# Kernel optimization log

Measured on AMD Instinct MI355X. Metric: run time of the kernel, lower is better.

## Reference

```python
import jax, jax.numpy as jnp
import numpy as np

UNITS = 128  # rnn_units hardcoded in the module


def setup_inputs() -> dict:
    key = jax.random.key(0)
    k1, k2, k3 = jax.random.split(key, 3)
    B, T, F = 256, 1024, 128  # feature dim must equal UNITS (shared cell across both layers)
    inputs = jax.random.normal(k1, (B, T, F), dtype=jnp.float32)
    # Keras LSTMCell params, gate order i|f|g|o; SHARED by both stacked layers
    # because StackedRNNCells([cell]*2) reuses the same cell object.
    W = jax.random.normal(k2, (F, 4 * UNITS), dtype=jnp.float32) * 0.05   # kernel
    U = jax.random.normal(k3, (UNITS, 4 * UNITS), dtype=jnp.float32) * 0.05  # recurrent_kernel
    b = jnp.zeros((4 * UNITS,), dtype=jnp.float32)  # bias
    return {"inputs": inputs, "W": W, "U": U, "b": b}


def _lstm_cell(x, h, c, W, U, b):
    # z: [B, 4*UNITS]; Keras gate order i, f, g(candidate), o
    z = x @ W + h @ U + b
    i, f, g, o = jnp.split(z, 4, axis=-1)
    i = jax.nn.sigmoid(i)
    f = jax.nn.sigmoid(f)
    g = jnp.tanh(g)
    o = jax.nn.sigmoid(o)
    c_new = f * c + i * g
    h_new = o * jnp.tanh(c_new)
    return h_new, c_new


def reference(inputs, W, U, b):
    B, T, F = inputs.shape
    z0 = jnp.zeros((B, UNITS), dtype=inputs.dtype)

    def step(carry, x_t):
        h1, c1, h2, c2 = carry
        h1, c1 = _lstm_cell(x_t, h1, c1, W, U, b)   # layer 1
        h2, c2 = _lstm_cell(h1, h2, c2, W, U, b)    # layer 2 (shared weights)
        return (h1, c1, h2, c2), None

    (h1, c1, h2, c2), _ = jax.lax.scan(step, (z0, z0, z0, z0), jnp.swapaxes(inputs, 0, 1))
    outputs = h2                                    # last-step output (return_sequences=False)
    init_state = jnp.zeros(inputs.shape, dtype=inputs.dtype)  # tf.zeros(inputs.shape)
    final_state = c1  # source unpacks `outputs, _, h2, _, _` -> 2nd flat state = layer-1 cell state
    return (outputs, init_state, final_state)
```

## Files before the change

### kernel.cpp

```cpp
#include <hip/hip_runtime.h>


typedef _Float16 f16;
typedef _Float16 f16x2 __attribute__((ext_vector_type(2)));
typedef _Float16 f16x8 __attribute__((ext_vector_type(8)));
typedef float    f32x4 __attribute__((ext_vector_type(4)));

#define T_STEPS 1024
#define UNITS   128
#define NLSTM   32
#define BPW     8
#define NBLK    256
#define OUT_ZERO 32768
#define OUT_C1   33587200
#define BUFB    6144

__device__ __forceinline__ float frcp_(float x) {
#if __has_builtin(__builtin_amdgcn_rcpf)
    return __builtin_amdgcn_rcpf(x);
#else
    return 1.0f / x;
#endif
}
__device__ __forceinline__ float sigmoidf_(float x) {
    return frcp_(1.0f + __expf(-x));
}
__device__ __forceinline__ float tanhf_(float x) {
    float e = __expf(2.0f * x);
    return 1.0f - 2.0f * frcp_(e + 1.0f);
}
__device__ __forceinline__ unsigned pkh(float a, float b) {
    f16x2 t; t[0] = (f16)a; t[1] = (f16)b;
    return __builtin_bit_cast(unsigned, t);
}

__global__ __launch_bounds__(512, 2) void lstm2_kernel(
    const float* __restrict__ X,
    const float* __restrict__ W,
    const float* __restrict__ U,
    const float* __restrict__ Bv,
    float* __restrict__ out)
{
    const int blk = blockIdx.x;
    const int tid = threadIdx.x;

    if (blk >= NLSTM) {
        const size_t nthr = (size_t)(NBLK - NLSTM) * 512;
        float4* dst = (float4*)(out + OUT_ZERO);
        const float4 z4 = make_float4(0.f, 0.f, 0.f, 0.f);
        for (size_t i = (size_t)(blk - NLSTM) * 512 + tid; i < 8388608u; i += nthr)
            dst[i] = z4;
        return;
    }

    const int w  = tid >> 6;
    const int l  = tid & 63;
    const int lr = l & 15;
    const int lc = l >> 4;
    const int u  = w * 16 + lr;
    const int b0 = blk * BPW;
    const bool cell2 = (l >= 32);
    const bool prio_wave = (w < 4);

    __shared__ __align__(16) char Abuf[2][BUFB];
    char* Ab = (char*)Abuf;

    f16x8 Wf[4][4], Uf[4][4];
    #pragma unroll
    for (int g = 0; g < 4; ++g) {
        #pragma unroll
        for (int kt = 0; kt < 4; ++kt) {
            f16x8 wt, ut;
            #pragma unroll
            for (int j = 0; j < 8; ++j) {
                const int krow = kt * 32 + lc * 8 + j;
                wt[j] = (f16)W[(size_t)krow * 512 + g * 128 + u];
                ut[j] = (f16)U[(size_t)krow * 512 + g * 128 + u];
            }
            Wf[g][kt] = wt;  Uf[g][kt] = ut;
        }
    }
    float bias[4];
    #pragma unroll
    for (int g = 0; g < 4; ++g) bias[g] = Bv[g * 128 + u];

    const int swz = (lr & 7) << 4;
    int raddr[2][4];
    #pragma unroll
    for (int a0 = 0; a0 < 2; ++a0)
        #pragma unroll
        for (int kt = 0; kt < 4; ++kt)
            raddr[a0][kt] = (((a0 * 8 + lr) * 256) + kt * 64 + lc * 16) ^ swz;
    int waddr[4];
    #pragma unroll
    for (int e = 0; e < 4; ++e)
        waddr[e] = ((8 + 4 * lc + e) * 256 + u * 2) ^ ((((4 * lc + e) & 7)) << 4);

    for (int i = tid; i < 3072; i += 512) ((float*)Ab)[i] = 0.0f;
    {
        const int flat = tid * 2, xr = flat >> 7, xc = flat & 127;
        const float2 xv = *(const float2*)(X + (size_t)(b0 + xr) * (T_STEPS * UNITS) + xc);
        const int byte = ((xr * 256 + xc * 2) ^ ((xr & 7) << 4));
        *(unsigned*)(Ab + byte) = pkh(xv.x, xv.y);
    }
    __syncthreads();

    float cst[4] = {0.f, 0.f, 0.f, 0.f};

    for (int k = 0; k <= T_STEPS; ++k) {
        const int rdo = (k & 1) * BUFB, wro = BUFB - rdo;

        float xa = 0.f, xb = 0.f; int xr = 0, xc = 0;
        if (k + 1 < T_STEPS) {
            const int flat = tid * 2; xr = flat >> 7; xc = flat & 127;
            const float2 xv = *(const float2*)(X + (size_t)(b0 + xr) * (T_STEPS * UNITS)
                                                 + (size_t)(k + 1) * UNITS + xc);
            xa = xv.x; xb = xv.y;
        }

        f16x8 A1[4], A2[4];
        #pragma unroll
        for (int kt = 0; kt < 4; ++kt) {
            A1[kt] = *(const f16x8*)(Ab + rdo + raddr[0][kt]);
            A2[kt] = *(const f16x8*)(Ab + rdo + raddr[1][kt]);
        }

        if (prio_wave) __builtin_amdgcn_s_setprio(1);
        f32x4 acc[4];
        #pragma unroll
        for (int g = 0; g < 4; ++g)
            acc[g] = f32x4{bias[g], bias[g], bias[g], bias[g]};
        #pragma unroll
        for (int kt = 0; kt < 4; ++kt)
            #pragma unroll
            for (int g = 0; g < 4; ++g)
                acc[g] = __builtin_amdgcn_mfma_f32_16x16x32_f16(A1[kt], Wf[g][kt], acc[g], 0, 0, 0);
        #pragma unroll
        for (int kt = 0; kt < 4; ++kt)
            #pragma unroll
            for (int g = 0; g < 4; ++g)
                acc[g] = __builtin_amdgcn_mfma_f32_16x16x32_f16(A2[kt], Uf[g][kt], acc[g], 0, 0, 0);
        if (prio_wave) __builtin_amdgcn_s_setprio(0);

        const bool active = cell2 ? (k > 0) : (k < T_STEPS);
        float hq[4];
        #pragma unroll
        for (int e = 0; e < 4; ++e) {
            const float ig = sigmoidf_(acc[0][e]);
            const float fg = sigmoidf_(acc[1][e]);
            const float gg = tanhf_(acc[2][e]);
            const float og = sigmoidf_(acc[3][e]);
            const float cn = fg * cst[e] + ig * gg;
            if (active) cst[e] = cn;
            hq[e] = og * tanhf_(cn);
        }

        if (active && k < T_STEPS) {
            #pragma unroll
            for (int e = 0; e < 4; ++e)
                *(f16*)(Ab + wro + waddr[e]) = (f16)hq[e];
        }
        if (k + 1 < T_STEPS) {
            const int byte = ((xr * 256 + xc * 2) ^ ((xr & 7) << 4));
            *(unsigned*)(Ab + wro + byte) = pkh(xa, xb);
        }

        if (k == T_STEPS - 1 && !cell2) {
            #pragma unroll
            for (int e = 0; e < 4; ++e)
                out[OUT_C1 + (size_t)(b0 + 4 * lc + e) * UNITS + u] = cst[e];
        }
        if (k == T_STEPS && cell2) {
            #pragma unroll
            for (int e = 0; e < 4; ++e)
                out[(size_t)(b0 + 4 * lc + e - 8) * UNITS + u] = hq[e];
        }
        __syncthreads();
    }
}

extern "C" void kernel_launch(void* const* d_in, const int* in_sizes, int n_in,
                              void* d_out, int out_size, void* d_ws, size_t ws_size,
                              hipStream_t stream) {
    const float* X  = (const float*)d_in[0];
    const float* W  = (const float*)d_in[1];
    const float* U  = (const float*)d_in[2];
    const float* Bv = (const float*)d_in[3];
    float* out = (float*)d_out;
    hipLaunchKernelGGL(lstm2_kernel, dim3(NBLK), dim3(512), 0, stream,
                       X, W, U, Bv, out);
}
```

Baseline: 1.207 ms.

## Split input projection out of recurrent path and batch x@W across two timesteps

Restructures the per-step MFMA schedule so the x@W input projection is computed ahead for two future timesteps at once on even steps, using a separate double-buffered x tile. The h@W product for layer 2 is shared via lane shuffles, and h@U is issued per gate, interleaved with the activation math. The goal is to shorten the serial dependency chain of each recurrent step and cut redundant MFMA work. In exchange the indexing and buffering become more complex, register pressure rises, and the old wave priority hints are dropped.

```diff
diff --git a/kernel.cpp b/kernel.cpp
--- a/kernel.cpp
+++ b/kernel.cpp
@@ -13,7 +13,8 @@
 #define NBLK    256
 #define OUT_ZERO 32768
 #define OUT_C1   33587200
-#define BUFB    6144
+
+#define MFMA16(A, B, C) __builtin_amdgcn_mfma_f32_16x16x32_f16((A), (B), (C), 0, 0, 0)
 
 __device__ __forceinline__ float frcp_(float x) {
 #if __has_builtin(__builtin_amdgcn_rcpf)
@@ -32,6 +33,9 @@
 __device__ __forceinline__ unsigned pkh(float a, float b) {
     f16x2 t; t[0] = (f16)a; t[1] = (f16)b;
     return __builtin_bit_cast(unsigned, t);
+}
+__device__ __forceinline__ int swb(int row, int byteoff) {
+    return row * 256 + (byteoff ^ ((row & 7) << 4));
 }
 
 __global__ __launch_bounds__(512, 2) void lstm2_kernel(
@@ -59,11 +63,11 @@
     const int lc = l >> 4;
     const int u  = w * 16 + lr;
     const int b0 = blk * BPW;
-    const bool cell2 = (l >= 32);
-    const bool prio_wave = (w < 4);
-
-    __shared__ __align__(16) char Abuf[2][BUFB];
-    char* Ab = (char*)Abuf;
+    const bool cell2 = (lc >= 2);
+    const size_t xstride = (size_t)(T_STEPS * UNITS);
+
+    __shared__ __align__(16) char hb[2][4096];
+    __shared__ __align__(16) char xb[2][4096];
 
     f16x8 Wf[4][4], Uf[4][4];
     #pragma unroll
@@ -84,85 +88,168 @@
     #pragma unroll
     for (int g = 0; g < 4; ++g) bias[g] = Bv[g * 128 + u];
 
-    const int swz = (lr & 7) << 4;
-    int raddr[2][4];
-    #pragma unroll
-    for (int a0 = 0; a0 < 2; ++a0)
-        #pragma unroll
-        for (int kt = 0; kt < 4; ++kt)
-            raddr[a0][kt] = (((a0 * 8 + lr) * 256) + kt * 64 + lc * 16) ^ swz;
-    int waddr[4];
-    #pragma unroll
-    for (int e = 0; e < 4; ++e)
-        waddr[e] = ((8 + 4 * lc + e) * 256 + u * 2) ^ ((((4 * lc + e) & 7)) << 4);
-
-    for (int i = tid; i < 3072; i += 512) ((float*)Ab)[i] = 0.0f;
+    int ard[4];
+    #pragma unroll
+    for (int kt = 0; kt < 4; ++kt) ard[kt] = swb(lr, kt * 64 + lc * 16);
+    int hwaddr[4];
+    #pragma unroll
+    for (int e = 0; e < 4; ++e) hwaddr[e] = swb(4 * lc + e, u * 2);
+
+    for (int i = tid; i < 2048; i += 512) ((float*)hb)[i] = 0.0f;
     {
-        const int flat = tid * 2, xr = flat >> 7, xc = flat & 127;
-        const float2 xv = *(const float2*)(X + (size_t)(b0 + xr) * (T_STEPS * UNITS) + xc);
-        const int byte = ((xr * 256 + xc * 2) ^ ((xr & 7) << 4));
-        *(unsigned*)(Ab + byte) = pkh(xv.x, xv.y);
+        const int r = tid >> 6, c = (tid & 63) * 2;
+        const float* Xb = X + (size_t)(b0 + r) * xstride + c;
+        const float2 v0 = *(const float2*)(Xb);
+        const float2 v1 = *(const float2*)(Xb + UNITS);
+        const float2 v2 = *(const float2*)(Xb + 2 * UNITS);
+        *(unsigned*)(&xb[1][0] + swb(r, c * 2))     = pkh(v0.x, v0.y);
+        *(unsigned*)(&xb[0][0] + swb(r, c * 2))     = pkh(v1.x, v1.y);
+        *(unsigned*)(&xb[0][0] + swb(8 + r, c * 2)) = pkh(v2.x, v2.y);
     }
     __syncthreads();
 
+    f32x4 accX[4];
+    {
+        f16x8 Ax[4];
+        #pragma unroll
+        for (int kt = 0; kt < 4; ++kt)
+            Ax[kt] = *(const f16x8*)(&xb[1][0] + swb(lr & 7, kt * 64 + lc * 16));
+        #pragma unroll
+        for (int g = 0; g < 4; ++g) accX[g] = f32x4{0.f, 0.f, 0.f, 0.f};
+        #pragma unroll
+        for (int kt = 0; kt < 4; ++kt)
+            #pragma unroll
+            for (int g = 0; g < 4; ++g)
+                accX[g] = MFMA16(Ax[kt], Wf[g][kt], accX[g]);
+    }
+    __syncthreads();
+
     float cst[4] = {0.f, 0.f, 0.f, 0.f};
 
     for (int k = 0; k <= T_STEPS; ++k) {
-        const int rdo = (k & 1) * BUFB, wro = BUFB - rdo;
-
-        float xa = 0.f, xb = 0.f; int xr = 0, xc = 0;
-        if (k + 1 < T_STEPS) {
-            const int flat = tid * 2; xr = flat >> 7; xc = flat & 127;
-            const float2 xv = *(const float2*)(X + (size_t)(b0 + xr) * (T_STEPS * UNITS)
-                                                 + (size_t)(k + 1) * UNITS + xc);
-            xa = xv.x; xb = xv.y;
-        }
-
-        f16x8 A1[4], A2[4];
-        #pragma unroll
-        for (int kt = 0; kt < 4; ++kt) {
-            A1[kt] = *(const f16x8*)(Ab + rdo + raddr[0][kt]);
-            A2[kt] = *(const f16x8*)(Ab + rdo + raddr[1][kt]);
-        }
-
-        if (prio_wave) __builtin_amdgcn_s_setprio(1);
-        f32x4 acc[4];
+        const int hrd = (k & 1) * 4096, hwr = 4096 - hrd;
+        const bool even = !(k & 1);
+        const bool runX = even && (k <= 1022);
+        const int xrd = ((k >> 1) & 1) * 4096;
+
+        const bool dir = (!even) || (k == 0);
+        float zxv[4][4];
         #pragma unroll
         for (int g = 0; g < 4; ++g)
-            acc[g] = f32x4{bias[g], bias[g], bias[g], bias[g]};
+            #pragma unroll
+            for (int e = 0; e < 4; ++e) {
+                const float v = accX[g][e];
+                const float s = __shfl_xor(v, 32);
+                zxv[g][e] = dir ? v : s;
+            }
+
+        const int m = k + 3;
+        const bool ldx = (m <= 1023);
+        const int xr = tid >> 6, xc = (tid & 63) * 2;
+        float2 xv = make_float2(0.f, 0.f);
+        if (ldx) xv = *(const float2*)(X + (size_t)(b0 + xr) * xstride + (size_t)m * UNITS + xc);
+
+        f16x8 Ah[4];
+        #pragma unroll
+        for (int kt = 0; kt < 4; ++kt)
+            Ah[kt] = *(const f16x8*)(&hb[0][0] + hrd + ard[kt]);
+        f16x8 Ax[4];
+        if (runX) {
+            #pragma unroll
+            for (int kt = 0; kt < 4; ++kt)
+                Ax[kt] = *(const f16x8*)(&xb[0][0] + xrd + ard[kt]);
+        }
+
+        f32x4 accW[4];
+        #pragma unroll
+        for (int g = 0; g < 4; ++g) accW[g] = f32x4{0.f, 0.f, 0.f, 0.f};
         #pragma unroll
         for (int kt = 0; kt < 4; ++kt)
             #pragma unroll
             for (int g = 0; g < 4; ++g)
-                acc[g] = __builtin_amdgcn_mfma_f32_16x16x32_f16(A1[kt], Wf[g][kt], acc[g], 0, 0, 0);
-        #pragma unroll
-        for (int kt = 0; kt < 4; ++kt)
-            #pragma unroll
-            for (int g = 0; g < 4; ++g)
-                acc[g] = __builtin_amdgcn_mfma_f32_16x16x32_f16(A2[kt], Uf[g][kt], acc[g], 0, 0, 0);
-        if (prio_wave) __builtin_amdgcn_s_setprio(0);
+                accW[g] = MFMA16(Ah[kt], Wf[g][kt], accW[g]);
+
+        f32x4 aug = {bias[2], bias[2], bias[2], bias[2]};
+        f32x4 auo = {bias[3], bias[3], bias[3], bias[3]};
+        float z2v[4][4];
+        aug = MFMA16(Ah[0], Uf[2][0], aug);  auo = MFMA16(Ah[0], Uf[3][0], auo);
+        z2v[0][0] = __shfl_xor(accW[0][0], 32);  z2v[0][1] = __shfl_xor(accW[0][1], 32);
+        z2v[0][2] = __shfl_xor(accW[0][2], 32);  z2v[0][3] = __shfl_xor(accW[0][3], 32);
+        aug = MFMA16(Ah[1], Uf[2][1], aug);  auo = MFMA16(Ah[1], Uf[3][1], auo);
+        z2v[1][0] = __shfl_xor(accW[1][0], 32);  z2v[1][1] = __shfl_xor(accW[1][1], 32);
+        z2v[1][2] = __shfl_xor(accW[1][2], 32);  z2v[1][3] = __shfl_xor(accW[1][3], 32);
+        aug = MFMA16(Ah[2], Uf[2][2], aug);  auo = MFMA16(Ah[2], Uf[3][2], auo);
+        z2v[2][0] = __shfl_xor(accW[2][0], 32);  z2v[2][1] = __shfl_xor(accW[2][1], 32);
+        z2v[2][2] = __shfl_xor(accW[2][2], 32);  z2v[2][3] = __shfl_xor(accW[2][3], 32);
+        aug = MFMA16(Ah[3], Uf[2][3], aug);  auo = MFMA16(Ah[3], Uf[3][3], auo);
+        z2v[3][0] = __shfl_xor(accW[3][0], 32);  z2v[3][1] = __shfl_xor(accW[3][1], 32);
+        z2v[3][2] = __shfl_xor(accW[3][2], 32);  z2v[3][3] = __shfl_xor(accW[3][3], 32);
+
+        f32x4 aui = {bias[0], bias[0], bias[0], bias[0]};
+        f32x4 auf = {bias[1], bias[1], bias[1], bias[1]};
+        float gg[4], oo[4];
+        aui = MFMA16(Ah[0], Uf[0][0], aui);  auf = MFMA16(Ah[0], Uf[1][0], auf);
+        { const float zg = aug[0] + (cell2 ? z2v[2][0] : zxv[2][0]); gg[0] = tanhf_(zg);
+          const float zo = auo[0] + (cell2 ? z2v[3][0] : zxv[3][0]); oo[0] = sigmoidf_(zo); }
+        aui = MFMA16(Ah[1], Uf[0][1], aui);  auf = MFMA16(Ah[1], Uf[1][1], auf);
+        { const float zg = aug[1] + (cell2 ? z2v[2][1] : zxv[2][1]); gg[1] = tanhf_(zg);
+          const float zo = auo[1] + (cell2 ? z2v[3][1] : zxv[3][1]); oo[1] = sigmoidf_(zo); }
+        aui = MFMA16(Ah[2], Uf[0][2], aui);  auf = MFMA16(Ah[2], Uf[1][2], auf);
+        { const float zg = aug[2] + (cell2 ? z2v[2][2] : zxv[2][2]); gg[2] = tanhf_(zg);
+          const float zo = auo[2] + (cell2 ? z2v[3][2] : zxv[3][2]); oo[2] = sigmoidf_(zo); }
+        aui = MFMA16(Ah[3], Uf[0][3], aui);  auf = MFMA16(Ah[3], Uf[1][3], auf);
+        { const float zg = aug[3] + (cell2 ? z2v[2][3] : zxv[2][3]); gg[3] = tanhf_(zg);
+          const float zo = auo[3] + (cell2 ? z2v[3][3] : zxv[3][3]); oo[3] = sigmoidf_(zo); }
 
         const bool active = cell2 ? (k > 0) : (k < T_STEPS);
+        float cn[4];
+        #pragma unroll
+        for (int e = 0; e < 4; ++e) {
+            const float zi = aui[e] + (cell2 ? z2v[0][e] : zxv[0][e]);
+            const float zf = auf[e] + (cell2 ? z2v[1][e] : zxv[1][e]);
+            const float ig = sigmoidf_(zi), fg = sigmoidf_(zf);
+            cn[e] = fg * cst[e] + ig * gg[e];
+            if (active) cst[e] = cn[e];
+        }
+
         float hq[4];
-        #pragma unroll
-        for (int e = 0; e < 4; ++e) {
-            const float ig = sigmoidf_(acc[0][e]);
-            const float fg = sigmoidf_(acc[1][e]);
-            const float gg = tanhf_(acc[2][e]);
-            const float og = sigmoidf_(acc[3][e]);
-            const float cn = fg * cst[e] + ig * gg;
-            if (active) cst[e] = cn;
-            hq[e] = og * tanhf_(cn);
+        if (runX) {
+            #pragma unroll
+            for (int g = 0; g < 4; ++g) accX[g] = f32x4{0.f, 0.f, 0.f, 0.f};
+            accX[0] = MFMA16(Ax[0], Wf[0][0], accX[0]);
+            accX[1] = MFMA16(Ax[0], Wf[1][0], accX[1]);
+            accX[2] = MFMA16(Ax[0], Wf[2][0], accX[2]);
+            accX[3] = MFMA16(Ax[0], Wf[3][0], accX[3]);
+            hq[0] = oo[0] * tanhf_(cn[0]);
+            accX[0] = MFMA16(Ax[1], Wf[0][1], accX[0]);
+            accX[1] = MFMA16(Ax[1], Wf[1][1], accX[1]);
+            accX[2] = MFMA16(Ax[1], Wf[2][1], accX[2]);
+            accX[3] = MFMA16(Ax[1], Wf[3][1], accX[3]);
+            hq[1] = oo[1] * tanhf_(cn[1]);
+            accX[0] = MFMA16(Ax[2], Wf[0][2], accX[0]);
+            accX[1] = MFMA16(Ax[2], Wf[1][2], accX[1]);
+            accX[2] = MFMA16(Ax[2], Wf[2][2], accX[2]);
+            accX[3] = MFMA16(Ax[2], Wf[3][2], accX[3]);
+            hq[2] = oo[2] * tanhf_(cn[2]);
+            accX[0] = MFMA16(Ax[3], Wf[0][3], accX[0]);
+            accX[1] = MFMA16(Ax[3], Wf[1][3], accX[1]);
+            accX[2] = MFMA16(Ax[3], Wf[2][3], accX[2]);
+            accX[3] = MFMA16(Ax[3], Wf[3][3], accX[3]);
+            hq[3] = oo[3] * tanhf_(cn[3]);
+        } else {
+            #pragma unroll
+            for (int e = 0; e < 4; ++e) hq[e] = oo[e] * tanhf_(cn[e]);
         }
 
         if (active && k < T_STEPS) {
             #pragma unroll
             for (int e = 0; e < 4; ++e)
-                *(f16*)(Ab + wro + waddr[e]) = (f16)hq[e];
-        }
-        if (k + 1 < T_STEPS) {
-            const int byte = ((xr * 256 + xc * 2) ^ ((xr & 7) << 4));
-            *(unsigned*)(Ab + wro + byte) = pkh(xa, xb);
+                *(f16*)(&hb[0][0] + hwr + hwaddr[e]) = (f16)hq[e];
+        }
+        if (ldx) {
+            const int row  = (m & 1) ? xr : (8 + xr);
+            const int slot = (m & 1) ? (((m - 1) >> 1) & 1) : (((m - 2) >> 1) & 1);
+            *(unsigned*)(&xb[0][0] + slot * 4096 + swb(row, xc * 2)) = pkh(xv.x, xv.y);
         }
 
         if (k == T_STEPS - 1 && !cell2) {
@@ -173,7 +260,7 @@
         if (k == T_STEPS && cell2) {
             #pragma unroll
             for (int e = 0; e < 4; ++e)
-                out[(size_t)(b0 + 4 * lc + e - 8) * UNITS + u] = hq[e];
+                out[(size_t)(b0 + 4 * (lc - 2) + e) * UNITS + u] = hq[e];
         }
         __syncthreads();
     }
```

Measured after the change: 2.189 ms. 1.81x slower.
